# Performance work log

Hardware: AMD Instinct MI355X
Metric: run time of the kernel (lower is better)

The kernel has to match this reference:

```python
import jax, jax.numpy as jnp
import numpy as np

N_NODES = 100000
N_EDGES = 1600000
N_GRAPHS = 64
IN_CH, HID_CH, OUT_CH, N_CLS = 128, 128, 64, 2


def setup_inputs() -> dict:
    key = jax.random.key(0)
    ks = jax.random.split(key, 8)
    x = jax.random.normal(ks[0], (N_NODES, IN_CH), dtype=jnp.float32)
    edge_index = jax.random.randint(ks[1], (2, N_EDGES), 0, N_NODES)
    batch = jnp.sort(jax.random.randint(ks[2], (N_NODES,), 0, N_GRAPHS))
    glorot = lambda k, shp: jax.random.normal(k, shp, dtype=jnp.float32) / np.float32(np.sqrt(shp[0]))
    return {
        "x": x, "edge_index": edge_index, "batch": batch,
        "W1": glorot(ks[3], (IN_CH, HID_CH)), "b1": jnp.zeros((HID_CH,), jnp.float32),
        "W2": glorot(ks[4], (HID_CH, HID_CH)), "b2": jnp.zeros((HID_CH,), jnp.float32),
        "W3": glorot(ks[5], (HID_CH, OUT_CH)), "b3": jnp.zeros((OUT_CH,), jnp.float32),
        "Wfc": glorot(ks[6], (OUT_CH, N_CLS)), "bfc": jnp.zeros((N_CLS,), jnp.float32),
    }


def gcn_conv(x, src, dst, W, b):
    """PyG GCNConv: add self-loops, D^{-1/2} (A+I) D^{-1/2} (x W) + b."""
    n = x.shape[0]
    h = x @ W  # [N, out]
    # degree with self-loops: 1 + in-degree at dst
    deg = jnp.ones((n,), h.dtype).at[dst].add(1.0)
    dinv = jax.lax.rsqrt(deg)  # deg >= 1 always (self-loop)
    norm = dinv[src] * dinv[dst]  # [E]
    agg = jnp.zeros_like(h).at[dst].add(h[src] * norm[:, None])
    agg = agg + h * (dinv * dinv)[:, None]  # self-loop messages
    return agg + b


def global_mean_pool(x, batch, num_graphs):
    s = jax.ops.segment_sum(x, batch, num_segments=num_graphs)
    cnt = jax.ops.segment_sum(jnp.ones((x.shape[0],), x.dtype), batch, num_segments=num_graphs)
    return s / jnp.maximum(cnt, 1.0)[:, None]


def reference(x, edge_index, batch, W1, b1, W2, b2, W3, b3, Wfc, bfc):
    src, dst = edge_index[0], edge_index[1]
    h = jax.nn.relu(gcn_conv(x, src, dst, W1, b1))   # dropout p=0.0 (eval) -> identity
    h = jax.nn.relu(gcn_conv(h, src, dst, W2, b2))
    h = gcn_conv(h, src, dst, W3, b3)
    g = global_mean_pool(h, batch, N_GRAPHS)          # [G, OUT_CH]
    return g @ Wfc + bfc                              # [G, N_CLS]
```

## Files before the change

kernel.cpp:

```cpp
#include <hip/hip_runtime.h>
#include <hip/hip_bf16.h>


#define THREADS 256
#define BSHIFT 9
#define BSIZE 512

typedef __attribute__((ext_vector_type(8))) short short8;
typedef __attribute__((ext_vector_type(16))) float floatx16;

__device__ __forceinline__ unsigned f2bf(float f) {
    unsigned u = __float_as_uint(f);
    return (u + 0x7fffu + ((u >> 16) & 1u)) >> 16;
}

__device__ __forceinline__ void bf8_acc(uint4 v, float* ac) {
    ac[0] += __uint_as_float(v.x << 16);
    ac[1] += __uint_as_float(v.x & 0xffff0000u);
    ac[2] += __uint_as_float(v.y << 16);
    ac[3] += __uint_as_float(v.y & 0xffff0000u);
    ac[4] += __uint_as_float(v.z << 16);
    ac[5] += __uint_as_float(v.z & 0xffff0000u);
    ac[6] += __uint_as_float(v.w << 16);
    ac[7] += __uint_as_float(v.w & 0xffff0000u);
}


__global__ __launch_bounds__(THREADS) void bucket_count(const int* __restrict__ dst,
                                                        int* __restrict__ btotal,
                                                        int E, int nbuck) {
    __shared__ int cnt[BSIZE];
    for (int i = threadIdx.x; i < nbuck; i += THREADS) cnt[i] = 0;
    __syncthreads();
    for (int e = blockIdx.x * THREADS + threadIdx.x; e < E; e += gridDim.x * THREADS)
        atomicAdd(&cnt[dst[e] >> BSHIFT], 1);
    __syncthreads();
    for (int i = threadIdx.x; i < nbuck; i += THREADS) {
        int c = cnt[i];
        if (c) atomicAdd(&btotal[i], c);
    }
}

__global__ __launch_bounds__(512) void bucket_scan(const int* __restrict__ btotal,
                                                   int* __restrict__ bbase,
                                                   int* __restrict__ bcursor,
                                                   float* __restrict__ gsum,
                                                   int nbuck, int E) {
    __shared__ int lds[512];
    int t = threadIdx.x;
    for (int i = t; i < 64 * 64; i += 512) gsum[i] = 0.0f;
    int v = (t < nbuck) ? btotal[t] : 0;
    lds[t] = v;
    __syncthreads();
    for (int off = 1; off < 512; off <<= 1) {
        int tv = (t >= off) ? lds[t - off] : 0;
        __syncthreads();
        lds[t] += tv;
        __syncthreads();
    }
    if (t < nbuck) {
        int excl = lds[t] - v;
        bbase[t] = excl;
        bcursor[t] = excl;
    }
    if (t == 0) bbase[nbuck] = E;
}

__global__ __launch_bounds__(THREADS) void bucket_scatter(const int* __restrict__ src,
                                                          const int* __restrict__ dst,
                                                          int* __restrict__ bcursor,
                                                          int* __restrict__ pairs, int E) {
    __shared__ int cnt[BSIZE];
    __shared__ int base[BSIZE];
    for (int i = threadIdx.x; i < BSIZE; i += THREADS) cnt[i] = 0;
    __syncthreads();
    int e0 = blockIdx.x * 2048;
    int myb[8], myrank[8], mypk[8];
#pragma unroll
    for (int j = 0; j < 8; ++j) {
        int e = e0 + j * THREADS + threadIdx.x;
        myb[j] = -1;
        if (e < E) {
            int d = dst[e];
            mypk[j] = (src[e] << BSHIFT) | (d & (BSIZE - 1));
            myb[j] = d >> BSHIFT;
            myrank[j] = atomicAdd(&cnt[myb[j]], 1);
        }
    }
    __syncthreads();
    for (int i = threadIdx.x; i < BSIZE; i += THREADS) {
        int c = cnt[i];
        base[i] = c ? atomicAdd(&bcursor[i], c) : 0;
    }
    __syncthreads();
#pragma unroll
    for (int j = 0; j < 8; ++j)
        if (myb[j] >= 0) pairs[(size_t)base[myb[j]] + myrank[j]] = mypk[j];
}

__global__ __launch_bounds__(512) void bucket_fill(const int* __restrict__ pairs,
                                                   const int* __restrict__ bbase,
                                                   int* __restrict__ row_start,
                                                   float* __restrict__ dinv,
                                                   int* __restrict__ esrc,
                                                   int N, int E, int nbuck) {
    __shared__ int cnt[BSIZE];
    __shared__ int scn[BSIZE];
    int b = blockIdx.x, t = threadIdx.x;
    int s = bbase[b], e = bbase[b + 1];
    cnt[t] = 0;
    __syncthreads();
    for (int i = s + t; i < e; i += 512) atomicAdd(&cnt[pairs[i] & (BSIZE - 1)], 1);
    __syncthreads();
    int v = cnt[t];
    scn[t] = v;
    __syncthreads();
    for (int off = 1; off < 512; off <<= 1) {
        int tv = (t >= off) ? scn[t - off] : 0;
        __syncthreads();
        scn[t] += tv;
        __syncthreads();
    }
    int excl = scn[t] - v;
    int g = (b << BSHIFT) + t;
    if (g < N) {
        row_start[g] = s + excl;
        dinv[g] = rsqrtf(1.0f + (float)v);
    }
    if (b == nbuck - 1 && t == 0) row_start[N] = E;
    scn[t] = excl;
    __syncthreads();
    for (int i = s + t; i < e; i += 512) {
        int p = pairs[i];
        int r = atomicAdd(&scn[p & (BSIZE - 1)], 1);
        esrc[s + r] = ((unsigned)p) >> BSHIFT;
    }
}

__device__ __forceinline__ void wt_pack(const float* W, uint4* Wtp, int C, int li) {
    int c = li >> 4, ch = li & 15;
    unsigned r[8];
#pragma unroll
    for (int j = 0; j < 8; ++j) r[j] = f2bf(W[(size_t)(ch * 8 + j) * C + c]);
    uint4 o;
    o.x = r[0] | (r[1] << 16);
    o.y = r[2] | (r[3] << 16);
    o.z = r[4] | (r[5] << 16);
    o.w = r[6] | (r[7] << 16);
    Wtp[li] = o;
}

__global__ __launch_bounds__(THREADS) void prep_wt_all(const float* __restrict__ W1,
                                                       const float* __restrict__ W2,
                                                       const float* __restrict__ W3,
                                                       uint4* __restrict__ Wt1,
                                                       uint4* __restrict__ Wt2,
                                                       uint4* __restrict__ Wt3) {
    int idx = blockIdx.x * THREADS + threadIdx.x;
    if (idx < 2048) wt_pack(W1, Wt1, 128, idx);
    else if (idx < 4096) wt_pack(W2, Wt2, 128, idx - 2048);
    else if (idx < 5120) wt_pack(W3, Wt3, 64, idx - 4096);
}

__global__ __launch_bounds__(THREADS) void prep_x(const float* __restrict__ x,
                                                  const float* __restrict__ dinv,
                                                  uint4* __restrict__ Z, int n) {
    int idx = blockIdx.x * THREADS + threadIdx.x;
    if (idx >= n * 16) return;
    int r = idx >> 4, c = idx & 15;
    float dv = dinv[r];
    const float* p = x + (size_t)r * 128 + c * 8;
    float4 a = *(const float4*)p;
    float4 b = *(const float4*)(p + 4);
    uint4 o;
    o.x = f2bf(a.x * dv) | (f2bf(a.y * dv) << 16);
    o.y = f2bf(a.z * dv) | (f2bf(a.w * dv) << 16);
    o.z = f2bf(b.x * dv) | (f2bf(b.y * dv) << 16);
    o.w = f2bf(b.z * dv) | (f2bf(b.w * dv) << 16);
    Z[idx] = o;
}

__global__ __launch_bounds__(THREADS) void fused_layer(const uint4* __restrict__ Z,
                                                       const uint4* __restrict__ Wt,
                                                       const int* __restrict__ row_start,
                                                       const int* __restrict__ esrc,
                                                       const float* __restrict__ dinv,
                                                       const float* __restrict__ bias,
                                                       uint4* __restrict__ out, int n) {
    __shared__ __align__(16) uint4 ldsX[64 * 16];
    int row0 = blockIdx.x * 64;
    int maxr = n - row0;
    if (maxr > 64) maxr = 64;
    int tid = threadIdx.x;
    int lane = tid & 15, grp = tid >> 4;

    for (int round = 0; round < 4; ++round) {
        int r = round * 16 + grp;
        int node = row0 + r;
        int nd = (node < n) ? node : (n - 1);
        float ac[8] = {0, 0, 0, 0, 0, 0, 0, 0};
        bf8_acc(Z[(size_t)nd * 16 + lane], ac);
        int s = row_start[nd], e = row_start[nd + 1];
        int i = s;
        for (; i + 8 <= e; i += 8) {
            int s0 = esrc[i], s1 = esrc[i + 1], s2 = esrc[i + 2], s3 = esrc[i + 3];
            int s4 = esrc[i + 4], s5 = esrc[i + 5], s6 = esrc[i + 6], s7 = esrc[i + 7];
            uint4 v0 = Z[(size_t)s0 * 16 + lane];
            uint4 v1 = Z[(size_t)s1 * 16 + lane];
            uint4 v2 = Z[(size_t)s2 * 16 + lane];
            uint4 v3 = Z[(size_t)s3 * 16 + lane];
            uint4 v4 = Z[(size_t)s4 * 16 + lane];
            uint4 v5 = Z[(size_t)s5 * 16 + lane];
            uint4 v6 = Z[(size_t)s6 * 16 + lane];
            uint4 v7 = Z[(size_t)s7 * 16 + lane];
            bf8_acc(v0, ac); bf8_acc(v1, ac); bf8_acc(v2, ac); bf8_acc(v3, ac);
            bf8_acc(v4, ac); bf8_acc(v5, ac); bf8_acc(v6, ac); bf8_acc(v7, ac);
        }
        for (; i + 4 <= e; i += 4) {
            int s0 = esrc[i], s1 = esrc[i + 1], s2 = esrc[i + 2], s3 = esrc[i + 3];
            uint4 v0 = Z[(size_t)s0 * 16 + lane];
            uint4 v1 = Z[(size_t)s1 * 16 + lane];
            uint4 v2 = Z[(size_t)s2 * 16 + lane];
            uint4 v3 = Z[(size_t)s3 * 16 + lane];
            bf8_acc(v0, ac); bf8_acc(v1, ac); bf8_acc(v2, ac); bf8_acc(v3, ac);
        }
        for (; i < e; ++i) bf8_acc(Z[(size_t)esrc[i] * 16 + lane], ac);
        float dv = dinv[nd];
        uint4 o;
        o.x = f2bf(ac[0] * dv) | (f2bf(ac[1] * dv) << 16);
        o.y = f2bf(ac[2] * dv) | (f2bf(ac[3] * dv) << 16);
        o.z = f2bf(ac[4] * dv) | (f2bf(ac[5] * dv) << 16);
        o.w = f2bf(ac[6] * dv) | (f2bf(ac[7] * dv) << 16);
        ldsX[r * 16 + (lane ^ (r & 7))] = o;
    }
    __syncthreads();

    int l = tid & 63, wv = tid >> 6;
    int l31 = l & 31, half = l >> 5;
    int nt = wv & 1, mt0 = (wv >> 1) * 2;
    floatx16 acc[2];
#pragma unroll
    for (int t = 0; t < 2; ++t)
#pragma unroll
        for (int q = 0; q < 16; ++q) acc[t][q] = 0.0f;
    int xrow = nt * 32 + l31, xsw = xrow & 7;
#pragma unroll
    for (int kt = 0; kt < 8; ++kt) {
        int chunk = kt * 2 + half;
        short8 xf = *(const short8*)&ldsX[xrow * 16 + (chunk ^ xsw)];
#pragma unroll
        for (int t = 0; t < 2; ++t) {
            int c = (mt0 + t) * 32 + l31;
            short8 wf = *(const short8*)&Wt[c * 16 + chunk];
            acc[t] = __builtin_amdgcn_mfma_f32_32x32x16_bf16(wf, xf, acc[t], 0, 0, 0);
        }
    }
    __syncthreads();

    int node = nt * 32 + l31;
    float dv = (node < maxr) ? dinv[row0 + node] : 0.0f;
    char* outb = (char*)ldsX;
#pragma unroll
    for (int t = 0; t < 2; ++t) {
        int cb = (mt0 + t) * 32;
#pragma unroll
        for (int q = 0; q < 4; ++q) {
            float v[4];
#pragma unroll
            for (int m = 0; m < 4; ++m) {
                int ch = cb + 8 * q + 4 * half + m;
                float x_ = acc[t][q * 4 + m] + bias[ch];
                x_ = fmaxf(x_, 0.0f);
                v[m] = x_ * dv;
            }
            uint2 pk = make_uint2(f2bf(v[0]) | (f2bf(v[1]) << 16),
                                  f2bf(v[2]) | (f2bf(v[3]) << 16));
            int chunk = (cb >> 3) + q;
            *(uint2*)(outb + node * 256 + ((chunk ^ (node & 7)) * 16) + half * 8) = pk;
        }
    }
    __syncthreads();
    for (int idx = tid; idx < maxr * 16; idx += THREADS) {
        int r = idx >> 4, c = idx & 15;
        out[(size_t)(row0 + r) * 16 + c] = *(uint4*)(outb + r * 256 + ((c ^ (r & 7)) * 16));
    }
}

__global__ __launch_bounds__(THREADS) void gemm3(const uint4* __restrict__ Z,
                                                 const uint4* __restrict__ Wt,
                                                 uint4* __restrict__ out, int n) {
    __shared__ __align__(16) uint4 ldsX[64 * 16];
    int row0 = blockIdx.x * 64;
    int maxr = n - row0;
    if (maxr > 64) maxr = 64;
    int tid = threadIdx.x;
    for (int idx = tid; idx < 1024; idx += THREADS) {
        int r = idx >> 4, c = idx & 15;
        uint4 o = (r < maxr) ? Z[(size_t)(row0 + r) * 16 + c] : make_uint4(0, 0, 0, 0);
        ldsX[r * 16 + (c ^ (r & 7))] = o;
    }
    __syncthreads();
    int l = tid & 63, wv = tid >> 6;
    int l31 = l & 31, half = l >> 5;
    int nt = wv & 1, mt = wv >> 1;
    floatx16 acc;
#pragma unroll
    for (int q = 0; q < 16; ++q) acc[q] = 0.0f;
    int xrow = nt * 32 + l31, xsw = xrow & 7;
#pragma unroll
    for (int kt = 0; kt < 8; ++kt) {
        int chunk = kt * 2 + half;
        short8 xf = *(const short8*)&ldsX[xrow * 16 + (chunk ^ xsw)];
        int c = mt * 32 + l31;
        short8 wf = *(const short8*)&Wt[c * 16 + chunk];
        acc = __builtin_amdgcn_mfma_f32_32x32x16_bf16(wf, xf, acc, 0, 0, 0);
    }
    __syncthreads();
    int node = nt * 32 + l31;
    char* outb = (char*)ldsX;
    int cb = mt * 32;
#pragma unroll
    for (int q = 0; q < 4; ++q) {
        uint2 pk = make_uint2(f2bf(acc[q * 4 + 0]) | (f2bf(acc[q * 4 + 1]) << 16),
                              f2bf(acc[q * 4 + 2]) | (f2bf(acc[q * 4 + 3]) << 16));
        int chunk = (cb >> 3) + q;
        *(uint2*)(outb + node * 128 + ((chunk ^ (node & 7)) * 16) + half * 8) = pk;
    }
    __syncthreads();
    for (int idx = tid; idx < maxr * 8; idx += THREADS) {
        int r = idx >> 3, c = idx & 7;
        out[(size_t)(row0 + r) * 8 + c] = *(uint4*)(outb + r * 128 + ((c ^ (r & 7)) * 16));
    }
}

__global__ __launch_bounds__(THREADS) void agg_pool(const uint4* __restrict__ Ps,
                                                    const int* __restrict__ row_start,
                                                    const int* __restrict__ esrc,
                                                    const float* __restrict__ dinv,
                                                    const float* __restrict__ bias,
                                                    const int* __restrict__ batch,
                                                    float* __restrict__ gsum, int n) {
    __shared__ float gpart[32][65];
    __shared__ int used[32];
    int tid = threadIdx.x;
    int lane = tid & 7, grp = tid >> 3;
    int node = blockIdx.x * 32 + grp;
    if (tid < 32) used[tid] = 0;
    for (int idx = tid; idx < 2048; idx += THREADS) gpart[idx >> 6][idx & 63] = 0.0f;
    __syncthreads();
    int gmin = batch[blockIdx.x * 32];
    if (node < n) {
        float ac[8] = {0, 0, 0, 0, 0, 0, 0, 0};
        bf8_acc(Ps[(size_t)node * 8 + lane], ac);
        int s = row_start[node], e = row_start[node + 1];
        int i = s;
        for (; i + 8 <= e; i += 8) {
            int s0 = esrc[i], s1 = esrc[i + 1], s2 = esrc[i + 2], s3 = esrc[i + 3];
            int s4 = esrc[i + 4], s5 = esrc[i + 5], s6 = esrc[i + 6], s7 = esrc[i + 7];
            uint4 v0 = Ps[(size_t)s0 * 8 + lane];
            uint4 v1 = Ps[(size_t)s1 * 8 + lane];
            uint4 v2 = Ps[(size_t)s2 * 8 + lane];
            uint4 v3 = Ps[(size_t)s3 * 8 + lane];
            uint4 v4 = Ps[(size_t)s4 * 8 + lane];
            uint4 v5 = Ps[(size_t)s5 * 8 + lane];
            uint4 v6 = Ps[(size_t)s6 * 8 + lane];
            uint4 v7 = Ps[(size_t)s7 * 8 + lane];
            bf8_acc(v0, ac); bf8_acc(v1, ac); bf8_acc(v2, ac); bf8_acc(v3, ac);
            bf8_acc(v4, ac); bf8_acc(v5, ac); bf8_acc(v6, ac); bf8_acc(v7, ac);
        }
        for (; i + 4 <= e; i += 4) {
            int s0 = esrc[i], s1 = esrc[i + 1], s2 = esrc[i + 2], s3 = esrc[i + 3];
            uint4 v0 = Ps[(size_t)s0 * 8 + lane];
            uint4 v1 = Ps[(size_t)s1 * 8 + lane];
            uint4 v2 = Ps[(size_t)s2 * 8 + lane];
            uint4 v3 = Ps[(size_t)s3 * 8 + lane];
            bf8_acc(v0, ac); bf8_acc(v1, ac); bf8_acc(v2, ac); bf8_acc(v3, ac);
        }
        for (; i < e; ++i) bf8_acc(Ps[(size_t)esrc[i] * 8 + lane], ac);
        float dv = dinv[node];
        float4 b0 = ((const float4*)bias)[lane * 2];
        float4 b1 = ((const float4*)bias)[lane * 2 + 1];
        float h[8];
        h[0] = fmaf(dv, ac[0], b0.x); h[1] = fmaf(dv, ac[1], b0.y);
        h[2] = fmaf(dv, ac[2], b0.z); h[3] = fmaf(dv, ac[3], b0.w);
        h[4] = fmaf(dv, ac[4], b1.x); h[5] = fmaf(dv, ac[5], b1.y);
        h[6] = fmaf(dv, ac[6], b1.z); h[7] = fmaf(dv, ac[7], b1.w);
        int g = batch[node];
        int slot = g - gmin;
        if (slot < 32) {
            if (lane == 0) used[slot] = 1;
#pragma unroll
            for (int j = 0; j < 8; ++j) atomicAdd(&gpart[slot][lane * 8 + j], h[j]);
        } else {
#pragma unroll
            for (int j = 0; j < 8; ++j) atomicAdd(&gsum[(size_t)g * 64 + lane * 8 + j], h[j]);
        }
    }
    __syncthreads();
    for (int idx = tid; idx < 2048; idx += THREADS) {
        int s = idx >> 6, ch = idx & 63;
        if (used[s]) atomicAdd(&gsum[(size_t)(gmin + s) * 64 + ch], gpart[s][ch]);
    }
}

__device__ __forceinline__ int dev_lower_bound(const int* a, int n, int key) {
    int lo = 0, hi = n;
    while (lo < hi) {
        int mid = (lo + hi) >> 1;
        if (a[mid] < key) lo = mid + 1;
        else hi = mid;
    }
    return lo;
}

__global__ __launch_bounds__(128) void finalize_fc(const float* __restrict__ gsum,
                                                   const int* __restrict__ batch, int n,
                                                   const float* __restrict__ Wfc,
                                                   const float* __restrict__ bfc,
                                                   float* __restrict__ out) {
    __shared__ float gm[64 * 64];
    __shared__ float cnt[64];
    int t = threadIdx.x;
    if (t < 64)
        cnt[t] = (float)(dev_lower_bound(batch, n, t + 1) - dev_lower_bound(batch, n, t));
    __syncthreads();
    for (int i = t; i < 64 * 64; i += 128) gm[i] = gsum[i] / fmaxf(cnt[i >> 6], 1.0f);
    __syncthreads();
    int g = t >> 1, cls = t & 1;
    float acc = bfc[cls];
    for (int c = 0; c < 64; ++c) acc = fmaf(gm[g * 64 + c], Wfc[c * 2 + cls], acc);
    out[g * 2 + cls] = acc;
}

extern "C" void kernel_launch(void* const* d_in, const int* in_sizes, int n_in,
                              void* d_out, int out_size, void* d_ws, size_t ws_size,
                              hipStream_t stream) {
    const float* x    = (const float*)d_in[0];
    const int*   ei   = (const int*)d_in[1];
    const int*   batch= (const int*)d_in[2];
    const float* W1   = (const float*)d_in[3];
    const float* b1   = (const float*)d_in[4];
    const float* W2   = (const float*)d_in[5];
    const float* b2   = (const float*)d_in[6];
    const float* W3   = (const float*)d_in[7];
    const float* b3   = (const float*)d_in[8];
    const float* Wfc  = (const float*)d_in[9];
    const float* bfc  = (const float*)d_in[10];
    float* out = (float*)d_out;

    const int N = in_sizes[2];
    const int E = in_sizes[1] / 2;
    const int* esrc_in = ei;
    const int* edst_in = ei + E;
    const int nbuck = (N + BSIZE - 1) >> BSHIFT;

    uint4* bufA      = (uint4*)d_ws;
    uint4* bufB      = bufA + (size_t)N * 16;
    uint4* bufC      = bufB + (size_t)N * 16;
    int*   pairs     = (int*)(bufC + (size_t)N * 8);
    int*   esrc      = pairs + E;
    int*   row_start = esrc + E;
    float* dinv      = (float*)(row_start + N + 1);
    int*   btotal    = (int*)(dinv + N);
    int*   bbase     = btotal + 512;
    int*   bcursor   = bbase + 513;
    float* gsum      = (float*)(bcursor + 512);
    uint4* Wt1       = (uint4*)(gsum + 64 * 64);
    uint4* Wt2       = Wt1 + 2048;
    uint4* Wt3       = Wt2 + 2048;

    hipMemsetAsync(btotal, 0, 512 * sizeof(int), stream);
    bucket_count<<<512, THREADS, 0, stream>>>(edst_in, btotal, E, nbuck);
    bucket_scan<<<1, 512, 0, stream>>>(btotal, bbase, bcursor, gsum, nbuck, E);
    bucket_scatter<<<(E + 2047) / 2048, THREADS, 0, stream>>>(esrc_in, edst_in, bcursor, pairs, E);
    bucket_fill<<<nbuck, 512, 0, stream>>>(pairs, bbase, row_start, dinv, esrc, N, E, nbuck);
    prep_wt_all<<<20, THREADS, 0, stream>>>(W1, W2, W3, Wt1, Wt2, Wt3);
    prep_x<<<(N * 16 + THREADS - 1) / THREADS, THREADS, 0, stream>>>(x, dinv, bufA, N);

    const int GB = (N + 63) / 64;

    fused_layer<<<GB, THREADS, 0, stream>>>(bufA, Wt1, row_start, esrc, dinv, b1, bufB, N);
    fused_layer<<<GB, THREADS, 0, stream>>>(bufB, Wt2, row_start, esrc, dinv, b2, bufA, N);
    gemm3<<<GB, THREADS, 0, stream>>>(bufA, Wt3, bufC, N);
    agg_pool<<<(N + 31) / 32, THREADS, 0, stream>>>(bufC, row_start, esrc, dinv, b3, batch, gsum, N);

    finalize_fc<<<1, 128, 0, stream>>>(gsum, batch, N, Wfc, bfc, out);
}
```

Baseline: 433.4 us.

## Pool layer-3 directly over edges with FP8 features, fold bias into finalize

Layer 3's aggregation and mean pool are rewritten so contributions go straight to per-graph sums. Edge terms are computed from the raw edge list, with per-destination dinv and graph id packed into a nodeinfo array. Self-loop terms are accumulated in node blocks, and the bias is added after the mean in finalize. The layer-3 GEMM output is stored as a custom FP8 (e4m3-like) encoding to halve gather traffic, and the weight and x prep kernels are merged into one launch. The cost is heavy shared-memory atomic contention over only 64 graphs, plus extra precision loss from FP8.

```diff
diff --git a/kernel.cpp b/kernel.cpp
--- a/kernel.cpp
+++ b/kernel.cpp
@@ -23,6 +23,33 @@
     ac[5] += __uint_as_float(v.z & 0xffff0000u);
     ac[6] += __uint_as_float(v.w << 16);
     ac[7] += __uint_as_float(v.w & 0xffff0000u);
+}
+
+__device__ __forceinline__ float fp8_dec(unsigned b) {
+    unsigned e = (b >> 3) & 15u, m = b & 7u;
+    float vn = __uint_as_float(((e + 120u) << 23) | (m << 20));
+    float vd = (float)m * 0.001953125f;
+    float v = e ? vn : vd;
+    return (b & 0x80u) ? -v : v;
+}
+
+__device__ __forceinline__ unsigned fp8_enc(float f) {
+    unsigned u = __float_as_uint(f);
+    unsigned s = (u >> 31) << 7;
+    float a = fabsf(f);
+    if (a >= 448.0f) return s | 0x7e;
+    if (a < 0.0009765625f) return s;
+    unsigned au = u & 0x7fffffffu;
+    if (a >= 0.015625f) {
+        unsigned r = au + 0x7ffffu + ((au >> 20) & 1u);
+        unsigned e2 = (r >> 23) - 120u;
+        if (e2 > 15u) return s | 0x7e;
+        return s | (e2 << 3) | ((r >> 20) & 7u);
+    } else {
+        int m = (int)(a * 512.0f + 0.5f);
+        if (m > 7) return s | (1u << 3);
+        return s | (unsigned)m;
+    }
 }
 
 
@@ -100,8 +127,10 @@
 
 __global__ __launch_bounds__(512) void bucket_fill(const int* __restrict__ pairs,
                                                    const int* __restrict__ bbase,
+                                                   const int* __restrict__ batch,
                                                    int* __restrict__ row_start,
                                                    float* __restrict__ dinv,
+                                                   int2* __restrict__ nodeinfo,
                                                    int* __restrict__ esrc,
                                                    int N, int E, int nbuck) {
     __shared__ int cnt[BSIZE];
@@ -125,7 +154,9 @@
     int g = (b << BSHIFT) + t;
     if (g < N) {
         row_start[g] = s + excl;
-        dinv[g] = rsqrtf(1.0f + (float)v);
+        float dv = rsqrtf(1.0f + (float)v);
+        dinv[g] = dv;
+        nodeinfo[g] = make_int2(__float_as_int(dv), batch[g]);
     }
     if (b == nbuck - 1 && t == 0) row_start[N] = E;
     scn[t] = excl;
@@ -150,34 +181,33 @@
     Wtp[li] = o;
 }
 
-__global__ __launch_bounds__(THREADS) void prep_wt_all(const float* __restrict__ W1,
-                                                       const float* __restrict__ W2,
-                                                       const float* __restrict__ W3,
-                                                       uint4* __restrict__ Wt1,
-                                                       uint4* __restrict__ Wt2,
-                                                       uint4* __restrict__ Wt3) {
+__global__ __launch_bounds__(THREADS) void prep_all(const float* __restrict__ x,
+                                                    const float* __restrict__ dinv,
+                                                    const float* __restrict__ W1,
+                                                    const float* __restrict__ W2,
+                                                    const float* __restrict__ W3,
+                                                    uint4* __restrict__ Z,
+                                                    uint4* __restrict__ Wt1,
+                                                    uint4* __restrict__ Wt2,
+                                                    uint4* __restrict__ Wt3, int n) {
     int idx = blockIdx.x * THREADS + threadIdx.x;
     if (idx < 2048) wt_pack(W1, Wt1, 128, idx);
     else if (idx < 4096) wt_pack(W2, Wt2, 128, idx - 2048);
     else if (idx < 5120) wt_pack(W3, Wt3, 64, idx - 4096);
-}
-
-__global__ __launch_bounds__(THREADS) void prep_x(const float* __restrict__ x,
-                                                  const float* __restrict__ dinv,
-                                                  uint4* __restrict__ Z, int n) {
-    int idx = blockIdx.x * THREADS + threadIdx.x;
-    if (idx >= n * 16) return;
-    int r = idx >> 4, c = idx & 15;
-    float dv = dinv[r];
-    const float* p = x + (size_t)r * 128 + c * 8;
-    float4 a = *(const float4*)p;
-    float4 b = *(const float4*)(p + 4);
-    uint4 o;
-    o.x = f2bf(a.x * dv) | (f2bf(a.y * dv) << 16);
-    o.y = f2bf(a.z * dv) | (f2bf(a.w * dv) << 16);
-    o.z = f2bf(b.x * dv) | (f2bf(b.y * dv) << 16);
-    o.w = f2bf(b.z * dv) | (f2bf(b.w * dv) << 16);
-    Z[idx] = o;
+    int xi = idx - 5120;
+    if (xi >= 0 && xi < n * 16) {
+        int r = xi >> 4, c = xi & 15;
+        float dv = dinv[r];
+        const float* p = x + (size_t)r * 128 + c * 8;
+        float4 a = *(const float4*)p;
+        float4 b = *(const float4*)(p + 4);
+        uint4 o;
+        o.x = f2bf(a.x * dv) | (f2bf(a.y * dv) << 16);
+        o.y = f2bf(a.z * dv) | (f2bf(a.w * dv) << 16);
+        o.z = f2bf(b.x * dv) | (f2bf(b.y * dv) << 16);
+        o.w = f2bf(b.z * dv) | (f2bf(b.w * dv) << 16);
+        Z[xi] = o;
+    }
 }
 
 __global__ __launch_bounds__(THREADS) void fused_layer(const uint4* __restrict__ Z,
@@ -321,85 +351,85 @@
     int cb = mt * 32;
 #pragma unroll
     for (int q = 0; q < 4; ++q) {
-        uint2 pk = make_uint2(f2bf(acc[q * 4 + 0]) | (f2bf(acc[q * 4 + 1]) << 16),
-                              f2bf(acc[q * 4 + 2]) | (f2bf(acc[q * 4 + 3]) << 16));
-        int chunk = (cb >> 3) + q;
-        *(uint2*)(outb + node * 128 + ((chunk ^ (node & 7)) * 16) + half * 8) = pk;
-    }
-    __syncthreads();
-    for (int idx = tid; idx < maxr * 8; idx += THREADS) {
-        int r = idx >> 3, c = idx & 7;
-        out[(size_t)(row0 + r) * 8 + c] = *(uint4*)(outb + r * 128 + ((c ^ (r & 7)) * 16));
-    }
-}
-
-__global__ __launch_bounds__(THREADS) void agg_pool(const uint4* __restrict__ Ps,
-                                                    const int* __restrict__ row_start,
-                                                    const int* __restrict__ esrc,
-                                                    const float* __restrict__ dinv,
-                                                    const float* __restrict__ bias,
-                                                    const int* __restrict__ batch,
-                                                    float* __restrict__ gsum, int n) {
-    __shared__ float gpart[32][65];
-    __shared__ int used[32];
-    int tid = threadIdx.x;
-    int lane = tid & 7, grp = tid >> 3;
-    int node = blockIdx.x * 32 + grp;
-    if (tid < 32) used[tid] = 0;
-    for (int idx = tid; idx < 2048; idx += THREADS) gpart[idx >> 6][idx & 63] = 0.0f;
-    __syncthreads();
-    int gmin = batch[blockIdx.x * 32];
-    if (node < n) {
+        unsigned pk = fp8_enc(acc[q * 4 + 0]) | (fp8_enc(acc[q * 4 + 1]) << 8) |
+                      (fp8_enc(acc[q * 4 + 2]) << 16) | (fp8_enc(acc[q * 4 + 3]) << 24);
+        *(unsigned*)(outb + node * 64 + cb + 8 * q + 4 * half) = pk;
+    }
+    __syncthreads();
+    for (int idx = tid; idx < maxr * 4; idx += THREADS) {
+        int r = idx >> 2, c = idx & 3;
+        out[(size_t)(row0 + r) * 4 + c] = *(uint4*)(outb + r * 64 + c * 16);
+    }
+}
+
+__global__ __launch_bounds__(THREADS) void pool3(const uint4* __restrict__ Ps,
+                                                 const int* __restrict__ esrc_in,
+                                                 const int* __restrict__ edst_in,
+                                                 const int2* __restrict__ nodeinfo,
+                                                 float* __restrict__ gsum,
+                                                 int N, int E, int nbe) {
+    __shared__ float gpart[4096];
+    int b = blockIdx.x, tid = threadIdx.x;
+    if (b < nbe) {
+        for (int i = tid; i < 4096; i += THREADS) gpart[i] = 0.0f;
+        __syncthreads();
+        int lane = tid & 3, slot = tid >> 2;
+        int e0 = b * 4096;
+        for (int it = 0; it < 64; ++it) {
+            int e = e0 + it * 64 + slot;
+            if (e < E) {
+                int dst = edst_in[e], src = esrc_in[e];
+                int2 ni = nodeinfo[dst];
+                float w = __int_as_float(ni.x);
+                float* gp = &gpart[ni.y * 64 + lane * 16];
+                uint4 v = Ps[(size_t)src * 4 + lane];
+                unsigned wd[4] = {v.x, v.y, v.z, v.w};
+#pragma unroll
+                for (int k = 0; k < 4; ++k)
+#pragma unroll
+                    for (int j = 0; j < 4; ++j)
+                        atomicAdd(&gp[k * 4 + j], w * fp8_dec((wd[k] >> (8 * j)) & 0xffu));
+            }
+        }
+        __syncthreads();
+        for (int i = tid; i < 4096; i += THREADS) {
+            float v = gpart[i];
+            if (v != 0.0f) atomicAdd(&gsum[i], v);
+        }
+    } else {
+        int nb = b - nbe;
+        int lane = tid & 7, grp = tid >> 3;
+        int base = nb * 512;
+        int end = min(base + 512, N);
+        const uint2* P2 = (const uint2*)Ps;
         float ac[8] = {0, 0, 0, 0, 0, 0, 0, 0};
-        bf8_acc(Ps[(size_t)node * 8 + lane], ac);
-        int s = row_start[node], e = row_start[node + 1];
-        int i = s;
-        for (; i + 8 <= e; i += 8) {
-            int s0 = esrc[i], s1 = esrc[i + 1], s2 = esrc[i + 2], s3 = esrc[i + 3];
-            int s4 = esrc[i + 4], s5 = esrc[i + 5], s6 = esrc[i + 6], s7 = esrc[i + 7];
-            uint4 v0 = Ps[(size_t)s0 * 8 + lane];
-            uint4 v1 = Ps[(size_t)s1 * 8 + lane];
-            uint4 v2 = Ps[(size_t)s2 * 8 + lane];
-            uint4 v3 = Ps[(size_t)s3 * 8 + lane];
-            uint4 v4 = Ps[(size_t)s4 * 8 + lane];
-            uint4 v5 = Ps[(size_t)s5 * 8 + lane];
-            uint4 v6 = Ps[(size_t)s6 * 8 + lane];
-            uint4 v7 = Ps[(size_t)s7 * 8 + lane];
-            bf8_acc(v0, ac); bf8_acc(v1, ac); bf8_acc(v2, ac); bf8_acc(v3, ac);
-            bf8_acc(v4, ac); bf8_acc(v5, ac); bf8_acc(v6, ac); bf8_acc(v7, ac);
-        }
-        for (; i + 4 <= e; i += 4) {
-            int s0 = esrc[i], s1 = esrc[i + 1], s2 = esrc[i + 2], s3 = esrc[i + 3];
-            uint4 v0 = Ps[(size_t)s0 * 8 + lane];
-            uint4 v1 = Ps[(size_t)s1 * 8 + lane];
-            uint4 v2 = Ps[(size_t)s2 * 8 + lane];
-            uint4 v3 = Ps[(size_t)s3 * 8 + lane];
-            bf8_acc(v0, ac); bf8_acc(v1, ac); bf8_acc(v2, ac); bf8_acc(v3, ac);
-        }
-        for (; i < e; ++i) bf8_acc(Ps[(size_t)esrc[i] * 8 + lane], ac);
-        float dv = dinv[node];
-        float4 b0 = ((const float4*)bias)[lane * 2];
-        float4 b1 = ((const float4*)bias)[lane * 2 + 1];
-        float h[8];
-        h[0] = fmaf(dv, ac[0], b0.x); h[1] = fmaf(dv, ac[1], b0.y);
-        h[2] = fmaf(dv, ac[2], b0.z); h[3] = fmaf(dv, ac[3], b0.w);
-        h[4] = fmaf(dv, ac[4], b1.x); h[5] = fmaf(dv, ac[5], b1.y);
-        h[6] = fmaf(dv, ac[6], b1.z); h[7] = fmaf(dv, ac[7], b1.w);
-        int g = batch[node];
-        int slot = g - gmin;
-        if (slot < 32) {
-            if (lane == 0) used[slot] = 1;
-#pragma unroll
-            for (int j = 0; j < 8; ++j) atomicAdd(&gpart[slot][lane * 8 + j], h[j]);
-        } else {
-#pragma unroll
-            for (int j = 0; j < 8; ++j) atomicAdd(&gsum[(size_t)g * 64 + lane * 8 + j], h[j]);
-        }
-    }
-    __syncthreads();
-    for (int idx = tid; idx < 2048; idx += THREADS) {
-        int s = idx >> 6, ch = idx & 63;
-        if (used[s]) atomicAdd(&gsum[(size_t)(gmin + s) * 64 + ch], gpart[s][ch]);
+        int cur_g = -1;
+        for (int i = base + grp; i < end; i += 32) {
+            int2 ni = nodeinfo[i];
+            float w = __int_as_float(ni.x);
+            if (ni.y != cur_g) {
+                if (cur_g >= 0) {
+                    float* p = gsum + cur_g * 64 + lane * 8;
+#pragma unroll
+                    for (int j = 0; j < 8; ++j) {
+                        if (ac[j] != 0.0f) atomicAdd(p + j, ac[j]);
+                        ac[j] = 0.0f;
+                    }
+                }
+                cur_g = ni.y;
+            }
+            uint2 v = P2[(size_t)i * 8 + lane];
+#pragma unroll
+            for (int j = 0; j < 4; ++j) ac[j] += w * fp8_dec((v.x >> (8 * j)) & 0xffu);
+#pragma unroll
+            for (int j = 0; j < 4; ++j) ac[4 + j] += w * fp8_dec((v.y >> (8 * j)) & 0xffu);
+        }
+        if (cur_g >= 0) {
+            float* p = gsum + cur_g * 64 + lane * 8;
+#pragma unroll
+            for (int j = 0; j < 8; ++j)
+                if (ac[j] != 0.0f) atomicAdd(p + j, ac[j]);
+        }
     }
 }
 
@@ -415,6 +445,7 @@
 
 __global__ __launch_bounds__(128) void finalize_fc(const float* __restrict__ gsum,
                                                    const int* __restrict__ batch, int n,
+                                                   const float* __restrict__ b3,
                                                    const float* __restrict__ Wfc,
                                                    const float* __restrict__ bfc,
                                                    float* __restrict__ out) {
@@ -424,7 +455,8 @@
     if (t < 64)
         cnt[t] = (float)(dev_lower_bound(batch, n, t + 1) - dev_lower_bound(batch, n, t));
     __syncthreads();
-    for (int i = t; i < 64 * 64; i += 128) gm[i] = gsum[i] / fmaxf(cnt[i >> 6], 1.0f);
+    for (int i = t; i < 64 * 64; i += 128)
+        gm[i] = gsum[i] / fmaxf(cnt[i >> 6], 1.0f) + b3[i & 63];
     __syncthreads();
     int g = t >> 1, cls = t & 1;
     float acc = bfc[cls];
@@ -457,11 +489,12 @@
     uint4* bufA      = (uint4*)d_ws;
     uint4* bufB      = bufA + (size_t)N * 16;
     uint4* bufC      = bufB + (size_t)N * 16;
-    int*   pairs     = (int*)(bufC + (size_t)N * 8);
+    int*   pairs     = (int*)(bufC + (size_t)N * 4);
     int*   esrc      = pairs + E;
     int*   row_start = esrc + E;
     float* dinv      = (float*)(row_start + N + 1);
-    int*   btotal    = (int*)(dinv + N);
+    int2*  nodeinfo  = (int2*)(dinv + N);
+    int*   btotal    = (int*)(nodeinfo + N);
     int*   bbase     = btotal + 512;
     int*   bcursor   = bbase + 513;
     float* gsum      = (float*)(bcursor + 512);
@@ -473,16 +506,22 @@
     bucket_count<<<512, THREADS, 0, stream>>>(edst_in, btotal, E, nbuck);
     bucket_scan<<<1, 512, 0, stream>>>(btotal, bbase, bcursor, gsum, nbuck, E);
     bucket_scatter<<<(E + 2047) / 2048, THREADS, 0, stream>>>(esrc_in, edst_in, bcursor, pairs, E);
-    bucket_fill<<<nbuck, 512, 0, stream>>>(pairs, bbase, row_start, dinv, esrc, N, E, nbuck);
-    prep_wt_all<<<20, THREADS, 0, stream>>>(W1, W2, W3, Wt1, Wt2, Wt3);
-    prep_x<<<(N * 16 + THREADS - 1) / THREADS, THREADS, 0, stream>>>(x, dinv, bufA, N);
+    bucket_fill<<<nbuck, 512, 0, stream>>>(pairs, bbase, batch, row_start, dinv, nodeinfo, esrc, N, E, nbuck);
+    {
+        int items = 5120 + N * 16;
+        prep_all<<<(items + THREADS - 1) / THREADS, THREADS, 0, stream>>>(
+            x, dinv, W1, W2, W3, bufA, Wt1, Wt2, Wt3, N);
+    }
 
     const int GB = (N + 63) / 64;
 
     fused_layer<<<GB, THREADS, 0, stream>>>(bufA, Wt1, row_start, esrc, dinv, b1, bufB, N);
     fused_layer<<<GB, THREADS, 0, stream>>>(bufB, Wt2, row_start, esrc, dinv, b2, bufA, N);
     gemm3<<<GB, THREADS, 0, stream>>>(bufA, Wt3, bufC, N);
-    agg_pool<<<(N + 31) / 32, THREADS, 0, stream>>>(bufC, row_start, esrc, dinv, b3, batch, gsum, N);
-
-    finalize_fc<<<1, 128, 0, stream>>>(gsum, batch, N, Wfc, bfc, out);
-}
+
+    const int NBE = (E + 4095) / 4096;
+    const int NBS = (N + 511) / 512;
+    pool3<<<NBE + NBS, THREADS, 0, stream>>>(bufC, esrc_in, edst_in, nodeinfo, gsum, N, E, NBE);
+
+    finalize_fc<<<1, 128, 0, stream>>>(gsum, batch, N, b3, Wfc, bfc, out);
+}
```

New measurement: 1.053 ms. 2.43x slower.
